# Kernel tuning notes

Measured on AMD Instinct MI355X. Metric: run time of the kernel, lower is better.

## Reference

```python
import math
import jax, jax.numpy as jnp
import numpy as np
from jax import lax

SQRT2 = math.sqrt(2.0)


def _conv2d(x, w, stride=1, padding=0):
    # x: [N,C,H,W], w: [O,I,kh,kw]
    return lax.conv_general_dilated(
        x, w,
        window_strides=(stride, stride),
        padding=[(padding, padding), (padding, padding)],
        dimension_numbers=('NCHW', 'OIHW', 'NCHW'))


def _fused_leaky_relu(x, bias, slope=0.2):
    # add per-channel bias, leaky relu, scale by sqrt(2) (StyleGAN2 FusedLeakyReLU)
    y = x + bias.reshape(1, -1, 1, 1)
    return jnp.where(y >= 0, y, slope * y) * SQRT2


def _upsample2x_bilinear(x):
    # matches torch F.interpolate(scale_factor=2, mode='bilinear', align_corners=False)
    n, c, h, w = x.shape
    return jax.image.resize(x, (n, c, 2 * h, 2 * w), method='bilinear')


def setup_inputs() -> dict:
    key = jax.random.key(0)
    k = jax.random.split(key, 5)
    Cin, Cout = 256, 128
    x = jax.random.normal(k[0], (8, Cin, 64, 64), dtype=jnp.float32)
    w1 = jax.random.normal(k[1], (Cin, Cin, 3, 3), dtype=jnp.float32)
    b1 = jnp.zeros((Cin,), dtype=jnp.float32)
    w2 = jax.random.normal(k[2], (Cout, Cin, 3, 3), dtype=jnp.float32)
    b2 = jnp.zeros((Cout,), dtype=jnp.float32)
    w_skip = jax.random.normal(k[3], (Cout, Cin, 1, 1), dtype=jnp.float32)
    return {"x": x, "w1": w1, "b1": b1, "w2": w2, "b2": b2, "w_skip": w_skip}


def reference(x, w1, b1, w2, b2, w_skip):
    Cin = x.shape[1]
    scale3 = 1.0 / math.sqrt(Cin * 9)  # equalized lr scale for 3x3
    scale1 = 1.0 / math.sqrt(Cin * 1)  # for 1x1 skip

    # conv1: EqualConv2d(in,in,3,pad=1,bias=False) + FusedLeakyReLU
    out = _conv2d(x, w1 * scale3, stride=1, padding=1)
    out = _fused_leaky_relu(out, b1)

    # conv2: bilinear up x2 + EqualConv(in,out,3,pad=1,no bias) + FusedLeakyReLU
    out = _upsample2x_bilinear(out)
    out = _conv2d(out, w2 * scale3, stride=1, padding=1)
    out = _fused_leaky_relu(out, b2)

    # skip: bilinear up x2 + 1x1 equalized conv, no bias/activation
    skip = _upsample2x_bilinear(x)
    skip = _conv2d(skip, w_skip * scale1, stride=1, padding=0)

    return (out + skip) / SQRT2
```

## Files before the change

### kernel.cpp

```cpp
#include <hip/hip_runtime.h>
#include <hip/hip_bf16.h>


typedef __attribute__((ext_vector_type(8))) short bf16x8;
typedef __attribute__((ext_vector_type(4))) float f32x4;

#define SQRT2F  1.41421356237309504880f
#define RSQRT2F 0.70710678118654752440f

__device__ __forceinline__ float lrelu_s(float v) { return v >= 0.f ? v : 0.2f * v; }

__device__ __forceinline__ unsigned short f2bf(float f) {
    unsigned u = __builtin_bit_cast(unsigned, f);
    u += 0x7fffu + ((u >> 16) & 1u);
    return (unsigned short)(u >> 16);
}
__device__ __forceinline__ float bflo(unsigned u) {
    return __builtin_bit_cast(float, u << 16);
}
__device__ __forceinline__ float bfhi(unsigned u) {
    return __builtin_bit_cast(float, u & 0xffff0000u);
}

__device__ __forceinline__ void up2_coef(int o, int lim, int& i0, int& i1, float& w0, float& w1) {
    int h = o >> 1;
    if (o & 1) { i0 = h; i1 = (h + 1 > lim) ? lim : h + 1; w0 = 0.75f; w1 = 0.25f; }
    else       { i0 = (h - 1 < 0) ? 0 : h - 1; i1 = h;     w0 = 0.25f; w1 = 0.75f; }
}

__global__ __launch_bounds__(256) void k_wtall(const float* __restrict__ w1,
                                               const float* __restrict__ w2,
                                               const float* __restrict__ wsk,
                                               unsigned short* __restrict__ w1T,
                                               unsigned short* __restrict__ w2T,
                                               unsigned short* __restrict__ wsT) {
    int i = blockIdx.x * 256 + threadIdx.x;
    if (i < 589824) {
        int cp  = i & 7;
        int t1i = i >> 3;  int ocp = t1i & 63;
        int t2i = t1i >> 6; int q  = t2i & 3;
        int t3  = t2i >> 2; int tap = t3 % 9;
        int t4  = t3 / 9;   int ci  = t4 & 7; int ocb = t4 >> 3;
        int oc = (ocb << 6) + ocp;
        int c  = (ci << 5) + (q << 3) + cp;
        w1T[i] = f2bf(w1[(oc * 256 + c) * 9 + tap] * (1.0f / 48.0f));
    } else if (i < 589824 + 294912) {
        int j = i - 589824;
        int cp  = j & 7;
        int t1i = j >> 3;  int ocp = t1i & 63;
        int t2i = t1i >> 6; int q  = t2i & 3;
        int t3  = t2i >> 2; int tap = t3 % 9;
        int t4  = t3 / 9;   int ci  = t4 & 7; int ocb = t4 >> 3;
        int oc = (ocb << 6) + ocp;
        int c  = (ci << 5) + (q << 3) + cp;
        w2T[j] = f2bf(w2[(oc * 256 + c) * 9 + tap] * (1.0f / 48.0f));
    } else if (i < 589824 + 294912 + 32768) {
        int j = i - (589824 + 294912);
        wsT[j] = f2bf(wsk[j] * (1.0f / 16.0f));
    }
}

__global__ __launch_bounds__(256) void k_xprep(const float* __restrict__ x,
                                               unsigned short* __restrict__ xT) {
    __shared__ float t[64][65];
    const int n = blockIdx.z, c0 = blockIdx.y << 6, p0 = blockIdx.x << 6;
    for (int i = threadIdx.x; i < 4096; i += 256) {
        int c = i >> 6, p = i & 63;
        t[c][p] = x[((size_t)(n * 256 + c0 + c) << 12) + p0 + p];
    }
    __syncthreads();
    for (int i = threadIdx.x; i < 4096; i += 256) {
        int p = i >> 6, c = i & 63;
        xT[((size_t)((n << 12) + p0 + p) << 8) + c0 + c] = f2bf(t[c][p]);
    }
}

__global__ __launch_bounds__(256, 2) void k_conv1(
    const unsigned short* __restrict__ xT, const unsigned short* __restrict__ w1T,
    const float* __restrict__ b1, unsigned short* __restrict__ t1)
{
    __shared__ __align__(16) unsigned short dt[6][66][40];
    __shared__ __align__(16) unsigned short wl[18432];
    const int tid = threadIdx.x;
    const int n   = blockIdx.x >> 4;
    const int y0  = (blockIdx.x & 15) << 2;
    const int ocb = blockIdx.y;
    const int oc0 = ocb << 6;
    const int w   = tid >> 6;
    const int m   = tid & 15;
    const int q   = (tid & 63) >> 4;

    f32x4 acc[4][4];
#pragma unroll
    for (int a = 0; a < 4; ++a)
#pragma unroll
        for (int g = 0; g < 4; ++g) acc[a][g] = (f32x4){0.f, 0.f, 0.f, 0.f};

    const unsigned short* wsrc = w1T + (size_t)ocb * 147456;
    const unsigned short* xTn  = xT + ((size_t)n << 20);
    unsigned short* dtf = &dt[0][0][0];

    int goff[7], ldsoff[7];
#pragma unroll
    for (int k = 0; k < 7; ++k) {
        int idx = tid + (k << 8);
        goff[k] = -1; ldsoff[k] = -1;
        if (idx < 1584) {
            int r = idx / 264; int rem = idx - r * 264; int col = rem >> 2; int g = rem & 3;
            ldsoff[k] = (r * 66 + col) * 40 + (g << 3);
            int gy = y0 - 1 + r, gx = col - 1;
            if ((unsigned)gy < 64u && (unsigned)gx < 64u)
                goff[k] = (((gy << 6) + gx) << 8) + (g << 3);
        }
    }

    uint4 vreg[7];
#pragma unroll
    for (int k = 0; k < 7; ++k) {
        vreg[k] = make_uint4(0, 0, 0, 0);
        if (goff[k] >= 0) vreg[k] = *(const uint4*)(xTn + goff[k]);
    }

    for (int ci = 0; ci < 8; ++ci) {
        uint4 twreg[9];
        const unsigned short* wc = wsrc + ci * 18432;
#pragma unroll
        for (int j = 0; j < 9; ++j)
            twreg[j] = *(const uint4*)(wc + ((tid + (j << 8)) << 3));
#pragma unroll
        for (int k = 0; k < 7; ++k)
            if (ldsoff[k] >= 0) *(uint4*)(dtf + ldsoff[k]) = vreg[k];
        if (ci < 7) {
            const int cn = (ci + 1) << 5;
#pragma unroll
            for (int k = 0; k < 7; ++k)
                if (goff[k] >= 0) vreg[k] = *(const uint4*)(xTn + goff[k] + cn);
        }
#pragma unroll
        for (int j = 0; j < 9; ++j)
            *(uint4*)(wl + ((tid + (j << 8)) << 3)) = twreg[j];
        __syncthreads();

        __builtin_amdgcn_s_setprio(1);
#pragma unroll
        for (int tap = 0; tap < 9; ++tap) {
            const int dy = tap / 3, dx = tap - 3 * (tap / 3);
            bf16x8 bfr[4];
#pragma unroll
            for (int g = 0; g < 4; ++g)
                bfr[g] = *(const bf16x8*)(&dt[w + dy][(g << 4) + m + dx][q << 3]);
#pragma unroll
            for (int a = 0; a < 4; ++a) {
                bf16x8 af = *(const bf16x8*)(wl + (((((tap << 2) + q) << 6) + (a << 4) + m) << 3));
#pragma unroll
                for (int g = 0; g < 4; ++g)
                    acc[a][g] = __builtin_amdgcn_mfma_f32_16x16x32_bf16(af, bfr[g], acc[a][g], 0, 0, 0);
            }
        }
        __builtin_amdgcn_s_setprio(0);
        __syncthreads();
    }

    const int y = y0 + w;
#pragma unroll
    for (int a = 0; a < 4; ++a) {
        const int oc = oc0 + (a << 4) + (q << 2);
        float b0 = b1[oc], b1v = b1[oc + 1], b2v = b1[oc + 2], b3 = b1[oc + 3];
#pragma unroll
        for (int g = 0; g < 4; ++g) {
            const int xcol = (g << 4) + m;
            unsigned lo = (unsigned)f2bf(lrelu_s(acc[a][g][0] + b0) * SQRT2F)
                        | ((unsigned)f2bf(lrelu_s(acc[a][g][1] + b1v) * SQRT2F) << 16);
            unsigned hi = (unsigned)f2bf(lrelu_s(acc[a][g][2] + b2v) * SQRT2F)
                        | ((unsigned)f2bf(lrelu_s(acc[a][g][3] + b3) * SQRT2F) << 16);
            uint2 s; s.x = lo; s.y = hi;
            *(uint2*)(t1 + (((n << 12) + (y << 6) + xcol) << 8) + oc) = s;
        }
    }
}

__global__ __launch_bounds__(256, 2) void k_skip(
    const unsigned short* __restrict__ xT, const unsigned short* __restrict__ wsT,
    unsigned short* __restrict__ t2)
{
    const int tid = threadIdx.x;
    const int w = tid >> 6, m = tid & 15, q = (tid & 63) >> 4;
    const int px0 = blockIdx.x << 6;
    const int apx = px0 + (w << 4) + m;

    f32x4 acc[8];
#pragma unroll
    for (int g = 0; g < 8; ++g) acc[g] = (f32x4){0.f, 0.f, 0.f, 0.f};

#pragma unroll
    for (int c0 = 0; c0 < 256; c0 += 32) {
        bf16x8 af = *(const bf16x8*)(xT + ((size_t)apx << 8) + c0 + (q << 3));
#pragma unroll
        for (int g = 0; g < 8; ++g) {
            bf16x8 bf = *(const bf16x8*)(wsT + (((g << 4) + m) << 8) + c0 + (q << 3));
            acc[g] = __builtin_amdgcn_mfma_f32_16x16x32_bf16(af, bf, acc[g], 0, 0, 0);
        }
    }
#pragma unroll
    for (int g = 0; g < 8; ++g) {
        const int oc = (g << 4) + m;
#pragma unroll
        for (int r = 0; r < 4; ++r) {
            int opx = px0 + (w << 4) + (q << 2) + r;
            t2[((size_t)opx << 7) + oc] = f2bf(acc[g][r]);
        }
    }
}

__global__ __launch_bounds__(256) void k_synthu(
    const unsigned short* __restrict__ t1, unsigned short* __restrict__ u)
{
    const int n = blockIdx.z, oy = blockIdx.y, x0 = blockIdx.x << 6;
    int ry0, ry1; float wy0, wy1;
    up2_coef(oy, 63, ry0, ry1, wy0, wy1);
    const unsigned short* tb = t1 + ((size_t)n << 20);
    unsigned short* ub = u + ((size_t)((n << 7) + oy) << 15);

    for (int idx = threadIdx.x; idx < 2048; idx += 256) {
        const int ox = x0 + (idx >> 5), g = idx & 31;
        int cx0, cx1; float wx0, wx1;
        up2_coef(ox, 63, cx0, cx1, wx0, wx1);
        const int co = g << 3;
        uint4 v00 = *(const uint4*)(tb + (((ry0 << 6) + cx0) << 8) + co);
        uint4 v01 = *(const uint4*)(tb + (((ry0 << 6) + cx1) << 8) + co);
        uint4 v10 = *(const uint4*)(tb + (((ry1 << 6) + cx0) << 8) + co);
        uint4 v11 = *(const uint4*)(tb + (((ry1 << 6) + cx1) << 8) + co);
        const unsigned* pa = (const unsigned*)&v00; const unsigned* pb = (const unsigned*)&v01;
        const unsigned* pc = (const unsigned*)&v10; const unsigned* pd = (const unsigned*)&v11;
        uint4 res; unsigned* pr = (unsigned*)&res;
#pragma unroll
        for (int j = 0; j < 4; ++j) {
            float vlo = wy0 * (wx0 * bflo(pa[j]) + wx1 * bflo(pb[j]))
                      + wy1 * (wx0 * bflo(pc[j]) + wx1 * bflo(pd[j]));
            float vhi = wy0 * (wx0 * bfhi(pa[j]) + wx1 * bfhi(pb[j]))
                      + wy1 * (wx0 * bfhi(pc[j]) + wx1 * bfhi(pd[j]));
            pr[j] = (unsigned)f2bf(vlo) | ((unsigned)f2bf(vhi) << 16);
        }
        *(uint4*)(ub + (ox << 8) + co) = res;
    }
}

__global__ __launch_bounds__(256, 2) void k_conv2u(
    const unsigned short* __restrict__ u, const unsigned short* __restrict__ w2T,
    const unsigned short* __restrict__ t2, const float* __restrict__ b2,
    float* __restrict__ out)
{
    __shared__ __align__(16) unsigned short dt[6][66][40];
    __shared__ __align__(16) unsigned short wl[18432];
    const int tid  = threadIdx.x;
    const int n    = blockIdx.x >> 6;
    const int rest = blockIdx.x & 63;
    const int oy0  = (rest >> 1) << 2;
    const int x0   = (rest & 1) << 6;
    const int ocb  = blockIdx.y;
    const int oc0  = ocb << 6;
    const int w    = tid >> 6;
    const int m    = tid & 15;
    const int q    = (tid & 63) >> 4;

    f32x4 acc[4][4];
#pragma unroll
    for (int a = 0; a < 4; ++a)
#pragma unroll
        for (int g = 0; g < 4; ++g) acc[a][g] = (f32x4){0.f, 0.f, 0.f, 0.f};

    const unsigned short* wsrc = w2T + (size_t)ocb * 147456;
    const unsigned short* ub   = u + ((size_t)n << 22);
    unsigned short* dtf = &dt[0][0][0];

    int goff[7], ldsoff[7];
#pragma unroll
    for (int k = 0; k < 7; ++k) {
        int idx = tid + (k << 8);
        goff[k] = -1; ldsoff[k] = -1;
        if (idx < 1584) {
            int r = idx / 264; int rem = idx - r * 264; int col = rem >> 2; int g = rem & 3;
            ldsoff[k] = (r * 66 + col) * 40 + (g << 3);
            int gy = oy0 - 1 + r, gx = x0 - 1 + col;
            if ((unsigned)gy < 128u && (unsigned)gx < 128u)
                goff[k] = (((gy << 7) + gx) << 8) + (g << 3);
        }
    }

    uint4 vreg[7];
#pragma unroll
    for (int k = 0; k < 7; ++k) {
        vreg[k] = make_uint4(0, 0, 0, 0);
        if (goff[k] >= 0) vreg[k] = *(const uint4*)(ub + goff[k]);
    }

    for (int ci = 0; ci < 8; ++ci) {
        uint4 twreg[9];
        const unsigned short* wc = wsrc + ci * 18432;
#pragma unroll
        for (int j = 0; j < 9; ++j)
            twreg[j] = *(const uint4*)(wc + ((tid + (j << 8)) << 3));
#pragma unroll
        for (int k = 0; k < 7; ++k)
            if (ldsoff[k] >= 0) *(uint4*)(dtf + ldsoff[k]) = vreg[k];
        if (ci < 7) {
            const int cn = (ci + 1) << 5;
#pragma unroll
            for (int k = 0; k < 7; ++k)
                if (goff[k] >= 0) vreg[k] = *(const uint4*)(ub + goff[k] + cn);
        }
#pragma unroll
        for (int j = 0; j < 9; ++j)
            *(uint4*)(wl + ((tid + (j << 8)) << 3)) = twreg[j];
        __syncthreads();

        __builtin_amdgcn_s_setprio(1);
#pragma unroll
        for (int tap = 0; tap < 9; ++tap) {
            const int dy = tap / 3, dx = tap - 3 * (tap / 3);
            bf16x8 bfr[4];
#pragma unroll
            for (int g = 0; g < 4; ++g)
                bfr[g] = *(const bf16x8*)(&dt[w + dy][(g << 4) + m + dx][q << 3]);
#pragma unroll
            for (int a = 0; a < 4; ++a) {
                bf16x8 af = *(const bf16x8*)(wl + (((((tap << 2) + q) << 6) + (a << 4) + m) << 3));
#pragma unroll
                for (int g = 0; g < 4; ++g)
                    acc[a][g] = __builtin_amdgcn_mfma_f32_16x16x32_bf16(af, bfr[g], acc[a][g], 0, 0, 0);
            }
        }
        __builtin_amdgcn_s_setprio(0);
        __syncthreads();
    }

    const int oy = oy0 + w;
    int ry0, ry1; float wy0, wy1;
    up2_coef(oy, 63, ry0, ry1, wy0, wy1);
    const unsigned short* t2b = t2 + ((size_t)n << 19);
#pragma unroll
    for (int a = 0; a < 4; ++a) {
        const int oc = oc0 + (a << 4) + (q << 2);
        float bb[4] = {b2[oc], b2[oc + 1], b2[oc + 2], b2[oc + 3]};
        float* pbase = out + ((size_t)(((n << 7) + oc) << 7) + oy) * 128;
#pragma unroll
        for (int g = 0; g < 4; ++g) {
            const int ox = x0 + (g << 4) + m;
            int cx0, cx1; float wx0, wx1;
            up2_coef(ox, 63, cx0, cx1, wx0, wx1);
            uint2 A = *(const uint2*)(t2b + (((ry0 << 6) + cx0) << 7) + oc);
            uint2 B = *(const uint2*)(t2b + (((ry0 << 6) + cx1) << 7) + oc);
            uint2 C = *(const uint2*)(t2b + (((ry1 << 6) + cx0) << 7) + oc);
            uint2 D = *(const uint2*)(t2b + (((ry1 << 6) + cx1) << 7) + oc);
            const unsigned* pA = (const unsigned*)&A; const unsigned* pB = (const unsigned*)&B;
            const unsigned* pC = (const unsigned*)&C; const unsigned* pD = (const unsigned*)&D;
#pragma unroll
            for (int r = 0; r < 4; ++r) {
                unsigned wa = pA[r >> 1], wb = pB[r >> 1], wc_ = pC[r >> 1], wd = pD[r >> 1];
                float va = (r & 1) ? bfhi(wa) : bflo(wa);
                float vb = (r & 1) ? bfhi(wb) : bflo(wb);
                float vc = (r & 1) ? bfhi(wc_) : bflo(wc_);
                float vd = (r & 1) ? bfhi(wd) : bflo(wd);
                float sk = wy0 * (wx0 * va + wx1 * vb) + wy1 * (wx0 * vc + wx1 * vd);
                pbase[(size_t)r * 16384 + ox] = lrelu_s(acc[a][g][r] + bb[r]) + sk * RSQRT2F;
            }
        }
    }
}

extern "C" void kernel_launch(void* const* d_in, const int* in_sizes, int n_in,
                              void* d_out, int out_size, void* d_ws, size_t ws_size,
                              hipStream_t stream)
{
    const float* x   = (const float*)d_in[0];
    const float* w1  = (const float*)d_in[1];
    const float* b1  = (const float*)d_in[2];
    const float* w2  = (const float*)d_in[3];
    const float* b2  = (const float*)d_in[4];
    const float* wsk = (const float*)d_in[5];
    float* out = (float*)d_out;

    unsigned short* xT  = (unsigned short*)d_ws;
    unsigned short* t1  = xT + 8388608;
    unsigned short* t2  = t1 + 8388608;
    unsigned short* w1T = t2 + 4194304;
    unsigned short* w2T = w1T + 589824;
    unsigned short* wsT = w2T + 294912;
    unsigned short* u   = wsT + 32768;

    k_wtall <<<dim3(3584), 256, 0, stream>>>(w1, w2, wsk, w1T, w2T, wsT);
    k_xprep <<<dim3(64, 4, 8), 256, 0, stream>>>(x, xT);
    k_conv1 <<<dim3(128, 4), 256, 0, stream>>>(xT, w1T, b1, t1);
    k_skip  <<<dim3(512), 256, 0, stream>>>(xT, wsT, t2);
    k_synthu<<<dim3(2, 128, 8), 256, 0, stream>>>(t1, u);
    k_conv2u<<<dim3(512, 2), 256, 0, stream>>>(u, w2T, t2, b2, out);
}
```

Before: 276.3 us.

## Merge prep and skip/upsample kernels; use channel-group-major LDS tile layout

The weight-transform and x-transpose kernels become one launch, and the skip 1x1 conv and the bilinear upsample synthesis become another, branching on block index. This cuts the launch count from six to four and lets independent work share the GPU. The LDS input tile for conv1 and conv2 changes from [row][col][40] padded rows to [channel-group][row][col][8], which is meant to give contiguous 16-byte fragment reads with fewer bank conflicts and less LDS. Merged kernels take the larger LDS and register footprint of either branch, which may lower occupancy for the lighter branch.

```diff
diff --git a/kernel.cpp b/kernel.cpp
--- a/kernel.cpp
+++ b/kernel.cpp
@@ -28,42 +28,45 @@
     else       { i0 = (h - 1 < 0) ? 0 : h - 1; i1 = h;     w0 = 0.25f; w1 = 0.75f; }
 }
 
-__global__ __launch_bounds__(256) void k_wtall(const float* __restrict__ w1,
-                                               const float* __restrict__ w2,
-                                               const float* __restrict__ wsk,
-                                               unsigned short* __restrict__ w1T,
-                                               unsigned short* __restrict__ w2T,
-                                               unsigned short* __restrict__ wsT) {
-    int i = blockIdx.x * 256 + threadIdx.x;
-    if (i < 589824) {
-        int cp  = i & 7;
-        int t1i = i >> 3;  int ocp = t1i & 63;
-        int t2i = t1i >> 6; int q  = t2i & 3;
-        int t3  = t2i >> 2; int tap = t3 % 9;
-        int t4  = t3 / 9;   int ci  = t4 & 7; int ocb = t4 >> 3;
-        int oc = (ocb << 6) + ocp;
-        int c  = (ci << 5) + (q << 3) + cp;
-        w1T[i] = f2bf(w1[(oc * 256 + c) * 9 + tap] * (1.0f / 48.0f));
-    } else if (i < 589824 + 294912) {
-        int j = i - 589824;
-        int cp  = j & 7;
-        int t1i = j >> 3;  int ocp = t1i & 63;
-        int t2i = t1i >> 6; int q  = t2i & 3;
-        int t3  = t2i >> 2; int tap = t3 % 9;
-        int t4  = t3 / 9;   int ci  = t4 & 7; int ocb = t4 >> 3;
-        int oc = (ocb << 6) + ocp;
-        int c  = (ci << 5) + (q << 3) + cp;
-        w2T[j] = f2bf(w2[(oc * 256 + c) * 9 + tap] * (1.0f / 48.0f));
-    } else if (i < 589824 + 294912 + 32768) {
-        int j = i - (589824 + 294912);
-        wsT[j] = f2bf(wsk[j] * (1.0f / 16.0f));
-    }
-}
-
-__global__ __launch_bounds__(256) void k_xprep(const float* __restrict__ x,
-                                               unsigned short* __restrict__ xT) {
+__global__ __launch_bounds__(256) void k_prep(const float* __restrict__ w1,
+                                              const float* __restrict__ w2,
+                                              const float* __restrict__ wsk,
+                                              const float* __restrict__ x,
+                                              unsigned short* __restrict__ w1T,
+                                              unsigned short* __restrict__ w2T,
+                                              unsigned short* __restrict__ wsT,
+                                              unsigned short* __restrict__ xT) {
     __shared__ float t[64][65];
-    const int n = blockIdx.z, c0 = blockIdx.y << 6, p0 = blockIdx.x << 6;
+    const int b = blockIdx.x;
+    if (b < 3584) {
+        int i = b * 256 + threadIdx.x;
+        if (i < 589824) {
+            int cp  = i & 7;
+            int t1i = i >> 3;  int ocp = t1i & 63;
+            int t2i = t1i >> 6; int q  = t2i & 3;
+            int t3  = t2i >> 2; int tap = t3 % 9;
+            int t4  = t3 / 9;   int ci  = t4 & 7; int ocb = t4 >> 3;
+            int oc = (ocb << 6) + ocp;
+            int c  = (ci << 5) + (q << 3) + cp;
+            w1T[i] = f2bf(w1[(oc * 256 + c) * 9 + tap] * (1.0f / 48.0f));
+        } else if (i < 589824 + 294912) {
+            int j = i - 589824;
+            int cp  = j & 7;
+            int t1i = j >> 3;  int ocp = t1i & 63;
+            int t2i = t1i >> 6; int q  = t2i & 3;
+            int t3  = t2i >> 2; int tap = t3 % 9;
+            int t4  = t3 / 9;   int ci  = t4 & 7; int ocb = t4 >> 3;
+            int oc = (ocb << 6) + ocp;
+            int c  = (ci << 5) + (q << 3) + cp;
+            w2T[j] = f2bf(w2[(oc * 256 + c) * 9 + tap] * (1.0f / 48.0f));
+        } else if (i < 589824 + 294912 + 32768) {
+            int j = i - (589824 + 294912);
+            wsT[j] = f2bf(wsk[j] * (1.0f / 16.0f));
+        }
+        return;
+    }
+    const int bb = b - 3584;
+    const int p0 = (bb & 63) << 6, c0 = ((bb >> 6) & 3) << 6, n = bb >> 8;
     for (int i = threadIdx.x; i < 4096; i += 256) {
         int c = i >> 6, p = i & 63;
         t[c][p] = x[((size_t)(n * 256 + c0 + c) << 12) + p0 + p];
@@ -79,7 +82,7 @@
     const unsigned short* __restrict__ xT, const unsigned short* __restrict__ w1T,
     const float* __restrict__ b1, unsigned short* __restrict__ t1)
 {
-    __shared__ __align__(16) unsigned short dt[6][66][40];
+    __shared__ __align__(16) unsigned short dt[4][6][66][8];
     __shared__ __align__(16) unsigned short wl[18432];
     const int tid = threadIdx.x;
     const int n   = blockIdx.x >> 4;
@@ -98,7 +101,7 @@
 
     const unsigned short* wsrc = w1T + (size_t)ocb * 147456;
     const unsigned short* xTn  = xT + ((size_t)n << 20);
-    unsigned short* dtf = &dt[0][0][0];
+    unsigned short* dtf = &dt[0][0][0][0];
 
     int goff[7], ldsoff[7];
 #pragma unroll
@@ -106,11 +109,11 @@
         int idx = tid + (k << 8);
         goff[k] = -1; ldsoff[k] = -1;
         if (idx < 1584) {
-            int r = idx / 264; int rem = idx - r * 264; int col = rem >> 2; int g = rem & 3;
-            ldsoff[k] = (r * 66 + col) * 40 + (g << 3);
+            int r = idx / 264; int rem = idx - r * 264; int col = rem >> 2; int cg = rem & 3;
+            ldsoff[k] = (cg * 396 + r * 66 + col) << 3;
             int gy = y0 - 1 + r, gx = col - 1;
             if ((unsigned)gy < 64u && (unsigned)gx < 64u)
-                goff[k] = (((gy << 6) + gx) << 8) + (g << 3);
+                goff[k] = (((gy << 6) + gx) << 8) + (cg << 3);
         }
     }
 
@@ -148,7 +151,7 @@
             bf16x8 bfr[4];
 #pragma unroll
             for (int g = 0; g < 4; ++g)
-                bfr[g] = *(const bf16x8*)(&dt[w + dy][(g << 4) + m + dx][q << 3]);
+                bfr[g] = *(const bf16x8*)(dtf + ((q * 396 + (w + dy) * 66 + (g << 4) + m + dx) << 3));
 #pragma unroll
             for (int a = 0; a < 4; ++a) {
                 bf16x8 af = *(const bf16x8*)(wl + (((((tap << 2) + q) << 6) + (a << 4) + m) << 3));
@@ -179,49 +182,50 @@
     }
 }
 
-__global__ __launch_bounds__(256, 2) void k_skip(
+__global__ __launch_bounds__(256, 2) void k_ss(
     const unsigned short* __restrict__ xT, const unsigned short* __restrict__ wsT,
-    unsigned short* __restrict__ t2)
+    const unsigned short* __restrict__ t1, unsigned short* __restrict__ t2,
+    unsigned short* __restrict__ u)
 {
+    const int b = blockIdx.x;
     const int tid = threadIdx.x;
-    const int w = tid >> 6, m = tid & 15, q = (tid & 63) >> 4;
-    const int px0 = blockIdx.x << 6;
-    const int apx = px0 + (w << 4) + m;
-
-    f32x4 acc[8];
-#pragma unroll
-    for (int g = 0; g < 8; ++g) acc[g] = (f32x4){0.f, 0.f, 0.f, 0.f};
-
-#pragma unroll
-    for (int c0 = 0; c0 < 256; c0 += 32) {
-        bf16x8 af = *(const bf16x8*)(xT + ((size_t)apx << 8) + c0 + (q << 3));
+    if (b < 512) {
+        const int w = tid >> 6, m = tid & 15, q = (tid & 63) >> 4;
+        const int px0 = b << 6;
+        const int apx = px0 + (w << 4) + m;
+
+        f32x4 acc[8];
+#pragma unroll
+        for (int g = 0; g < 8; ++g) acc[g] = (f32x4){0.f, 0.f, 0.f, 0.f};
+
+#pragma unroll
+        for (int c0 = 0; c0 < 256; c0 += 32) {
+            bf16x8 af = *(const bf16x8*)(xT + ((size_t)apx << 8) + c0 + (q << 3));
+#pragma unroll
+            for (int g = 0; g < 8; ++g) {
+                bf16x8 bf = *(const bf16x8*)(wsT + (((g << 4) + m) << 8) + c0 + (q << 3));
+                acc[g] = __builtin_amdgcn_mfma_f32_16x16x32_bf16(af, bf, acc[g], 0, 0, 0);
+            }
+        }
 #pragma unroll
         for (int g = 0; g < 8; ++g) {
-            bf16x8 bf = *(const bf16x8*)(wsT + (((g << 4) + m) << 8) + c0 + (q << 3));
-            acc[g] = __builtin_amdgcn_mfma_f32_16x16x32_bf16(af, bf, acc[g], 0, 0, 0);
-        }
-    }
-#pragma unroll
-    for (int g = 0; g < 8; ++g) {
-        const int oc = (g << 4) + m;
-#pragma unroll
-        for (int r = 0; r < 4; ++r) {
-            int opx = px0 + (w << 4) + (q << 2) + r;
-            t2[((size_t)opx << 7) + oc] = f2bf(acc[g][r]);
-        }
-    }
-}
-
-__global__ __launch_bounds__(256) void k_synthu(
-    const unsigned short* __restrict__ t1, unsigned short* __restrict__ u)
-{
-    const int n = blockIdx.z, oy = blockIdx.y, x0 = blockIdx.x << 6;
+            const int oc = (g << 4) + m;
+#pragma unroll
+            for (int r = 0; r < 4; ++r) {
+                int opx = px0 + (w << 4) + (q << 2) + r;
+                t2[((size_t)opx << 7) + oc] = f2bf(acc[g][r]);
+            }
+        }
+        return;
+    }
+    const int bb = b - 512;
+    const int n = bb >> 8, oy = (bb >> 1) & 127, x0 = (bb & 1) << 6;
     int ry0, ry1; float wy0, wy1;
     up2_coef(oy, 63, ry0, ry1, wy0, wy1);
     const unsigned short* tb = t1 + ((size_t)n << 20);
     unsigned short* ub = u + ((size_t)((n << 7) + oy) << 15);
 
-    for (int idx = threadIdx.x; idx < 2048; idx += 256) {
+    for (int idx = tid; idx < 2048; idx += 256) {
         const int ox = x0 + (idx >> 5), g = idx & 31;
         int cx0, cx1; float wx0, wx1;
         up2_coef(ox, 63, cx0, cx1, wx0, wx1);
@@ -250,7 +254,7 @@
     const unsigned short* __restrict__ t2, const float* __restrict__ b2,
     float* __restrict__ out)
 {
-    __shared__ __align__(16) unsigned short dt[6][66][40];
+    __shared__ __align__(16) unsigned short dt[4][6][66][8];
     __shared__ __align__(16) unsigned short wl[18432];
     const int tid  = threadIdx.x;
     const int n    = blockIdx.x >> 6;
@@ -271,7 +275,7 @@
 
     const unsigned short* wsrc = w2T + (size_t)ocb * 147456;
     const unsigned short* ub   = u + ((size_t)n << 22);
-    unsigned short* dtf = &dt[0][0][0];
+    unsigned short* dtf = &dt[0][0][0][0];
 
     int goff[7], ldsoff[7];
 #pragma unroll
@@ -279,11 +283,11 @@
         int idx = tid + (k << 8);
         goff[k] = -1; ldsoff[k] = -1;
         if (idx < 1584) {
-            int r = idx / 264; int rem = idx - r * 264; int col = rem >> 2; int g = rem & 3;
-            ldsoff[k] = (r * 66 + col) * 40 + (g << 3);
+            int r = idx / 264; int rem = idx - r * 264; int col = rem >> 2; int cg = rem & 3;
+            ldsoff[k] = (cg * 396 + r * 66 + col) << 3;
             int gy = oy0 - 1 + r, gx = x0 - 1 + col;
             if ((unsigned)gy < 128u && (unsigned)gx < 128u)
-                goff[k] = (((gy << 7) + gx) << 8) + (g << 3);
+                goff[k] = (((gy << 7) + gx) << 8) + (cg << 3);
         }
     }
 
@@ -321,7 +325,7 @@
             bf16x8 bfr[4];
 #pragma unroll
             for (int g = 0; g < 4; ++g)
-                bfr[g] = *(const bf16x8*)(&dt[w + dy][(g << 4) + m + dx][q << 3]);
+                bfr[g] = *(const bf16x8*)(dtf + ((q * 396 + (w + dy) * 66 + (g << 4) + m + dx) << 3));
 #pragma unroll
             for (int a = 0; a < 4; ++a) {
                 bf16x8 af = *(const bf16x8*)(wl + (((((tap << 2) + q) << 6) + (a << 4) + m) << 3));
@@ -388,10 +392,8 @@
     unsigned short* wsT = w2T + 294912;
     unsigned short* u   = wsT + 32768;
 
-    k_wtall <<<dim3(3584), 256, 0, stream>>>(w1, w2, wsk, w1T, w2T, wsT);
-    k_xprep <<<dim3(64, 4, 8), 256, 0, stream>>>(x, xT);
+    k_prep  <<<dim3(5632), 256, 0, stream>>>(w1, w2, wsk, x, w1T, w2T, wsT, xT);
     k_conv1 <<<dim3(128, 4), 256, 0, stream>>>(xT, w1T, b1, t1);
-    k_skip  <<<dim3(512), 256, 0, stream>>>(xT, wsT, t2);
-    k_synthu<<<dim3(2, 128, 8), 256, 0, stream>>>(t1, u);
+    k_ss    <<<dim3(2560), 256, 0, stream>>>(xT, wsT, t1, t2, u);
     k_conv2u<<<dim3(512, 2), 256, 0, stream>>>(u, w2T, t2, b2, out);
 }
```

New measurement: 267.6 us. -3.1%, faster.
